# Performance work log

Measured on AMD Instinct MI355X. Metric: run time of the kernel, lower is better.

Reference implementation:

```python
import jax, jax.numpy as jnp
import numpy as np

B, N, D = 8, 64, 512          # batch, latent tokens, token dim
C, H, W, P = 256, 128, 128, 36  # img feat channels/HW, sampling points
PG = 128                       # parameter-generator inner dim (0.25*D)
HEADS = 8                      # D // 64
TOT = C * C + P * P            # adaptive mixing param count per token


def _ln(x, g, b):
    m = x.mean(-1, keepdims=True)
    v = x.var(-1, keepdims=True)
    return (x - m) / jnp.sqrt(v + 1e-5) * g + b


def _gelu(x):
    return jax.nn.gelu(x, approximate=False)


def _grid_sample(img, grid):
    # img: (B,C,H,W); grid: (B,N,P,2) in [-1,1]; bilinear, border pad, align_corners=False
    Bi, Ci, Hi, Wi = img.shape
    x = ((grid[..., 0] + 1.0) * Wi - 1.0) * 0.5
    y = ((grid[..., 1] + 1.0) * Hi - 1.0) * 0.5
    x0 = jnp.floor(x)
    y0 = jnp.floor(y)
    wx = x - x0
    wy = y - y0
    x0i = jnp.clip(x0.astype(jnp.int32), 0, Wi - 1)
    x1i = jnp.clip(x0.astype(jnp.int32) + 1, 0, Wi - 1)
    y0i = jnp.clip(y0.astype(jnp.int32), 0, Hi - 1)
    y1i = jnp.clip(y0.astype(jnp.int32) + 1, 0, Hi - 1)
    imgt = img.transpose(0, 2, 3, 1)  # (B,H,W,C)
    bidx = jnp.arange(Bi)[:, None, None]
    v00 = imgt[bidx, y0i, x0i]  # (B,N,P,C)
    v01 = imgt[bidx, y0i, x1i]
    v10 = imgt[bidx, y1i, x0i]
    v11 = imgt[bidx, y1i, x1i]
    wx = wx[..., None]
    wy = wy[..., None]
    return (v00 * (1 - wx) * (1 - wy) + v01 * wx * (1 - wy)
            + v10 * (1 - wx) * wy + v11 * wx * wy)


def setup_inputs() -> dict:
    key = jax.random.key(0)
    ks = jax.random.split(key, 16)
    rn = lambda k, s, sc: jax.random.normal(k, s, jnp.float32) * sc
    tl = jax.random.uniform(ks[0], (B, N, 2), jnp.float32) * 0.5
    wh = 0.2 + jax.random.uniform(ks[1], (B, N, 2), jnp.float32) * 0.4
    return dict(
        token_embed=rn(ks[2], (B, N, D), 1.0),
        token_roi=jnp.concatenate([tl, tl + wh], axis=-1),
        img_feat=rn(ks[3], (B, C, H, W), 1.0),
        ln_off_g=jnp.ones(D), ln_off_b=jnp.zeros(D),
        w_off=rn(ks[4], (D, P * 2), D ** -0.5),
        roi_offset_bias=rn(ks[5], (P * 2,), 1.0),
        ln_pg_g=jnp.ones(D), ln_pg_b=jnp.zeros(D),
        w_pg1=rn(ks[6], (D, PG), D ** -0.5), b_pg1=jnp.zeros(PG),
        w_pg2=rn(ks[7], (PG, TOT), 0.02 * PG ** -0.5),
        b_pg2=rn(ks[8], (TOT,), 0.02),
        m_beta=jnp.zeros(C), s_beta=jnp.zeros(P),
        w_out=rn(ks[9], (P * C, D), (P * C) ** -0.5), b_out=jnp.zeros(D),
        ln1_g=jnp.ones(D), ln1_b=jnp.zeros(D),
        w_qkv=rn(ks[10], (D, 3 * D), D ** -0.5), b_qkv=jnp.zeros(3 * D),
        w_proj=rn(ks[11], (D, D), D ** -0.5), b_proj=jnp.zeros(D),
        ln2_g=jnp.ones(D), ln2_b=jnp.zeros(D),
        w_fc1=rn(ks[12], (D, 4 * D), D ** -0.5), b_fc1=jnp.zeros(4 * D),
        w_fc2=rn(ks[13], (4 * D, D), (4 * D) ** -0.5), b_fc2=jnp.zeros(D),
    )


def reference(token_embed, token_roi, img_feat,
              ln_off_g, ln_off_b, w_off, roi_offset_bias,
              ln_pg_g, ln_pg_b, w_pg1, b_pg1, w_pg2, b_pg2,
              m_beta, s_beta, w_out, b_out,
              ln1_g, ln1_b, w_qkv, b_qkv, w_proj, b_proj,
              ln2_g, ln2_b, w_fc1, b_fc1, w_fc2, b_fc2):
    Bq, Nq, Dm = token_embed.shape
    # --- OP.SAMPLING_M: offsets -> absolute points (n_heads=1) ---
    off = _ln(token_embed, ln_off_g, ln_off_b) @ w_off + roi_offset_bias  # (B,N,2P)
    off = off.reshape(Bq, Nq, 1, P, 2)
    mu = off.mean(-2, keepdims=True)
    sd = jnp.std(off, axis=-2, keepdims=True, ddof=1) + 1e-5  # unbiased, as torch.std
    off = (off - mu) / (3.0 * sd)
    xy = (token_roi[..., 2:] + token_roi[..., :2]) * 0.5
    wh = token_roi[..., 2:] - token_roi[..., :2]
    pts = xy[:, :, None, None, :] + off * wh[:, :, None, None, :]  # (B,N,1,P,2)
    grid = pts.reshape(Bq, Nq, P, 2) * 2.0 - 1.0
    sampled = _grid_sample(img_feat, grid)  # (B,N,P,C)
    # --- adaptive mixing (AdaMixer): per-token generated channel/spatial weights ---
    q = _ln(token_embed, ln_pg_g, ln_pg_b)
    params = (q @ w_pg1 + b_pg1) @ w_pg2 + b_pg2  # (B,N,TOT)
    cm = params[..., :C * C].reshape(Bq, Nq, C, C)
    sm = params[..., C * C:].reshape(Bq, Nq, P, P)
    h = _gelu(jnp.einsum('bnpc,bncd->bnpd', sampled, cm) + m_beta)
    h = _gelu(jnp.einsum('bnqp,bnpd->bnqd', sm, h) + s_beta[:, None])
    token_embed = token_embed + (h.reshape(Bq, Nq, P * C) @ w_out + b_out)
    # --- OP.ATTN ---
    x = _ln(token_embed, ln1_g, ln1_b)
    hd = Dm // HEADS
    qkv = (x @ w_qkv + b_qkv).reshape(Bq, Nq, 3, HEADS, hd)
    qh, kh, vh = qkv[:, :, 0], qkv[:, :, 1], qkv[:, :, 2]
    att = jax.nn.softmax(jnp.einsum('bqhd,bkhd->bhqk', qh, kh) * hd ** -0.5, axis=-1)
    o = jnp.einsum('bhqk,bkhd->bqhd', att, vh).reshape(Bq, Nq, Dm)
    token_embed = token_embed + (o @ w_proj + b_proj)
    # --- OP.MLP ---
    x = _ln(token_embed, ln2_g, ln2_b)
    token_embed = token_embed + (_gelu(x @ w_fc1 + b_fc1) @ w_fc2 + b_fc2)
    return token_embed
```

## Files before the change

kernel.cpp:

```cpp
#include <hip/hip_runtime.h>
#include <hip/hip_bf16.h>

typedef __hip_bfloat16 bf16;
typedef __attribute__((ext_vector_type(8))) short short8;
typedef __attribute__((ext_vector_type(4))) short s16x4;
typedef __attribute__((ext_vector_type(4))) float f32x4;

#define NTOK 512
#define TOTC 66832
#define CM_SZ 65536

__device__ __forceinline__ float b2f(bf16 x) { return __bfloat162float(x); }
__device__ __forceinline__ bf16 f2b(float x) { return __float2bfloat16(x); }
__device__ __forceinline__ float gelu_f(float x) {
  return 0.5f * x * (1.0f + erff(x * 0.7071067811865476f));
}
__device__ __forceinline__ f32x4 mfma16(short8 a, short8 b, f32x4 c) {
  return __builtin_amdgcn_mfma_f32_16x16x32_bf16(a, b, c, 0, 0, 0);
}

__global__ __launch_bounds__(256) void k_head(
    const float* __restrict__ te, const float* __restrict__ roi,
    const float* __restrict__ g_off, const float* __restrict__ b_off,
    const float* __restrict__ w_off, const float* __restrict__ off_bias,
    const float* __restrict__ g_pg, const float* __restrict__ b_pg,
    const float* __restrict__ w_pg1, const float* __restrict__ b_pg1,
    bf16* __restrict__ t_out, int* __restrict__ meta_i, float* __restrict__ meta_w,
    const float* __restrict__ img, bf16* __restrict__ imgT,
    const float* __restrict__ w0, bf16* __restrict__ o0,
    const float* __restrict__ w1, bf16* __restrict__ o1,
    const float* __restrict__ w2, bf16* __restrict__ o2,
    const float* __restrict__ w3, bf16* __restrict__ o3,
    const float* __restrict__ w4, bf16* __restrict__ o4) {
  __shared__ __align__(16) char smem_raw[36864];
  int blk = blockIdx.x;
  int t = threadIdx.x;
  if (blk < 512) {
    int tok = blk;
    int lane = t & 63, w = t >> 6;
    float* xo = (float*)smem_raw;
    float* xq = xo + 512;
    float* offb = xq + 512;
    float* red = offb + 72;
    float* wsum = red + 4;
    size_t base = (size_t)tok * 512;
    float a0 = te[base + t];
    float a1 = te[base + t + 256];
    float s = a0 + a1;
#pragma unroll
    for (int o = 32; o; o >>= 1) s += __shfl_xor(s, o);
    if (lane == 0) wsum[w] = s;
    __syncthreads();
    float mean = (wsum[0] + wsum[1] + wsum[2] + wsum[3]) * (1.0f / 512.0f);
    float d0 = a0 - mean, d1 = a1 - mean;
    float ss = d0 * d0 + d1 * d1;
#pragma unroll
    for (int o = 32; o; o >>= 1) ss += __shfl_xor(ss, o);
    __syncthreads();
    if (lane == 0) wsum[w] = ss;
    __syncthreads();
    float var = (wsum[0] + wsum[1] + wsum[2] + wsum[3]) * (1.0f / 512.0f);
    float rstd = rsqrtf(var + 1e-5f);
    xo[t] = d0 * rstd * g_off[t] + b_off[t];
    xo[t + 256] = d1 * rstd * g_off[t + 256] + b_off[t + 256];
    xq[t] = d0 * rstd * g_pg[t] + b_pg[t];
    xq[t + 256] = d1 * rstd * g_pg[t + 256] + b_pg[t + 256];
    __syncthreads();
    if (t < 128) {
      float acc = b_pg1[t];
      for (int d = 0; d < 512; ++d) acc = fmaf(xq[d], w_pg1[d * 128 + t], acc);
      t_out[(size_t)tok * 128 + t] = f2b(acc);
    } else if (t < 200) {
      int j = t - 128;
      float acc = off_bias[j];
      for (int d = 0; d < 512; ++d) acc = fmaf(xo[d], w_off[d * 72 + j], acc);
      offb[j] = acc;
    }
    __syncthreads();
    if (t < 2) {
      float mu = 0.f;
      for (int p = 0; p < 36; ++p) mu += offb[p * 2 + t];
      mu *= (1.0f / 36.0f);
      float s2 = 0.f;
      for (int p = 0; p < 36; ++p) { float dd = offb[p * 2 + t] - mu; s2 += dd * dd; }
      float sd = sqrtf(s2 * (1.0f / 35.0f)) + 1e-5f;
      red[t] = mu;
      red[2 + t] = 1.0f / (3.0f * sd);
    }
    __syncthreads();
    if (t < 36) {
      int p = t;
      float r0 = roi[tok * 4 + 0], r1 = roi[tok * 4 + 1];
      float r2 = roi[tok * 4 + 2], r3 = roi[tok * 4 + 3];
      float cx = (r0 + r2) * 0.5f, cy = (r1 + r3) * 0.5f;
      float bw = r2 - r0, bh = r3 - r1;
      float ox = (offb[p * 2 + 0] - red[0]) * red[2];
      float oy = (offb[p * 2 + 1] - red[1]) * red[3];
      float fx = (cx + ox * bw) * 128.0f - 0.5f;
      float fy = (cy + oy * bh) * 128.0f - 0.5f;
      float x0f = floorf(fx), y0f = floorf(fy);
      float wx = fx - x0f, wy = fy - y0f;
      int x0 = min(max((int)x0f, 0), 127);
      int x1 = min(max((int)x0f + 1, 0), 127);
      int y0 = min(max((int)y0f, 0), 127);
      int y1 = min(max((int)y0f + 1, 0), 127);
      int ibase = (tok >> 6) * 16384;
      int mi = (tok * 36 + p) * 4;
      meta_i[mi + 0] = (ibase + y0 * 128 + x0) * 256;
      meta_i[mi + 1] = (ibase + y0 * 128 + x1) * 256;
      meta_i[mi + 2] = (ibase + y1 * 128 + x0) * 256;
      meta_i[mi + 3] = (ibase + y1 * 128 + x1) * 256;
      meta_w[mi + 0] = (1.f - wx) * (1.f - wy);
      meta_w[mi + 1] = wx * (1.f - wy);
      meta_w[mi + 2] = (1.f - wx) * wy;
      meta_w[mi + 3] = wx * wy;
    }
  } else if (blk < 2560) {
    int bb = blk - 512;
    int b = bb >> 8;
    int hw0 = (bb & 255) * 64;
    bf16 (*tl)[72] = (bf16(*)[72])smem_raw;
    int hw_l = (t & 15) * 4;
#pragma unroll
    for (int pass = 0; pass < 16; ++pass) {
      int c = (t >> 4) + 16 * pass;
      const float4 v = *(const float4*)&img[((size_t)(b * 256 + c) << 14) + hw0 + hw_l];
      float vv[4] = {v.x, v.y, v.z, v.w};
      int mask = ((c >> 3) & 31) << 1;
      int base = hw_l ^ (mask & 60);
      int swp = mask & 2;
      bf16 o[4];
#pragma unroll
      for (int k = 0; k < 4; ++k) o[k] = f2b(vv[k ^ swp]);
      *(s16x4*)&tl[c][base] = *(const s16x4*)o;
    }
    __syncthreads();
    int c8 = (t & 31) * 8;
    int hwb = t >> 5;
    int rmask = ((c8 >> 3) & 31) << 1;
#pragma unroll
    for (int pass = 0; pass < 8; ++pass) {
      int hw = hwb + 8 * pass;
      bf16 tmp[8];
#pragma unroll
      for (int j = 0; j < 8; ++j) tmp[j] = tl[c8 + j][hw ^ rmask];
      *(short8*)&imgT[((size_t)(b << 14) + hw0 + hw) * 256 + c8] = *(const short8*)tmp;
    }
  } else {
    int b = blk - 2560;
    const float* W;
    bf16* O;
    int K, N, loc;
    if (b < 4608) { W = w0; O = o0; K = 9216; N = 512; loc = b; }
    else if (b < 5376) { W = w1; O = o1; K = 512; N = 1536; loc = b - 4608; }
    else if (b < 5632) { W = w2; O = o2; K = 512; N = 512; loc = b - 5376; }
    else if (b < 6656) { W = w3; O = o3; K = 512; N = 2048; loc = b - 5632; }
    else { W = w4; O = o4; K = 2048; N = 512; loc = b - 6656; }
    int ntn = N >> 5;
    int nb = loc % ntn, kb = loc / ntn;
    int n0 = nb * 32, k0 = kb * 32;
    float (*tw)[33] = (float(*)[33])smem_raw;
    int r = t >> 5, c = t & 31;
#pragma unroll
    for (int i = 0; i < 4; ++i)
      tw[r + 8 * i][c] = W[(size_t)(k0 + r + 8 * i) * N + n0 + c];
    __syncthreads();
    int n_l = t >> 3, k4 = (t & 7) * 4;
    bf16 tmp[4];
#pragma unroll
    for (int j = 0; j < 4; ++j) tmp[j] = f2b(tw[k4 + j][n_l]);
    *(s16x4*)&O[(size_t)(n0 + n_l) * K + k0 + k4] = *(const s16x4*)tmp;
  }
}

__global__ __launch_bounds__(256) void k_samp_pg2(
    const bf16* __restrict__ tb16, const float* __restrict__ w2,
    const float* __restrict__ b2, bf16* __restrict__ pchunk,
    const bf16* __restrict__ imgT, const int* __restrict__ meta_i,
    const float* __restrict__ meta_w, bf16* __restrict__ S) {
  __shared__ bf16 BsT[64][136];
  __shared__ bf16 stg[64][72];
  int blk = blockIdx.x;
  int t = threadIdx.x;
  if (blk < 1045) {
    int n0 = blk * 64;
    int lane = t & 63, w = t >> 6;
    int quad = lane >> 4, l16 = lane & 15;
    {
      int nl = (t & 15) * 4, kk = t >> 4;
#pragma unroll
      for (int pass = 0; pass < 8; ++pass) {
        int k = kk + pass * 16;
        int n = n0 + nl;
        int nc = (n + 3 < TOTC) ? n : (TOTC - 4);
        const float4 v = *(const float4*)(w2 + (size_t)k * TOTC + nc);
        BsT[nl + 0][k] = f2b(v.x);
        BsT[nl + 1][k] = f2b(v.y);
        BsT[nl + 2][k] = f2b(v.z);
        BsT[nl + 3][k] = f2b(v.w);
      }
    }
    __syncthreads();
    float bias_r[4];
#pragma unroll
    for (int nt = 0; nt < 4; ++nt) {
      int col = n0 + nt * 16 + l16;
      bias_r[nt] = (col < TOTC) ? b2[col] : 0.f;
    }
    for (int half = 0; half < 2; ++half) {
      int row0 = half * 256;
      f32x4 acc[4][4];
#pragma unroll
      for (int i = 0; i < 4; ++i)
#pragma unroll
        for (int j = 0; j < 4; ++j) acc[i][j] = (f32x4){0.f, 0.f, 0.f, 0.f};
      const bf16* Abase = tb16 + ((size_t)(row0 + w * 64 + l16)) * 128 + quad * 8;
#pragma unroll
      for (int ks = 0; ks < 4; ++ks) {
        short8 af[4], bff[4];
#pragma unroll
        for (int mt = 0; mt < 4; ++mt)
          af[mt] = *(const short8*)(Abase + mt * 16 * 128 + ks * 32);
#pragma unroll
        for (int nt = 0; nt < 4; ++nt)
          bff[nt] = *(const short8*)(&BsT[nt * 16 + l16][ks * 32 + quad * 8]);
#pragma unroll
        for (int mt = 0; mt < 4; ++mt)
#pragma unroll
          for (int nt = 0; nt < 4; ++nt)
            acc[mt][nt] = mfma16(af[mt], bff[nt], acc[mt][nt]);
      }
#pragma unroll
      for (int mt = 0; mt < 4; ++mt) {
        __syncthreads();
#pragma unroll
        for (int nt = 0; nt < 4; ++nt)
#pragma unroll
          for (int r = 0; r < 4; ++r)
            stg[w * 16 + quad * 4 + r][nt * 16 + l16] =
                f2b(acc[mt][nt][r] + bias_r[nt]);
        __syncthreads();
#pragma unroll
        for (int pass = 0; pass < 2; ++pass) {
          int t2 = t + pass * 256;
          int row_l = t2 >> 3;
          int wi = row_l >> 4, rr = row_l & 15;
          int c8 = (t2 & 7) * 8;
          int col = n0 + c8;
          if (col < TOTC) {
            int grow = row0 + wi * 64 + mt * 16 + rr;
            *(short8*)&pchunk[(size_t)grow * TOTC + col] =
                *(const short8*)&stg[wi * 16 + rr][c8];
          }
        }
      }
      __syncthreads();
    }
  } else {
    int tok = blk - 1045;
#pragma unroll 6
    for (int p = 0; p < 36; ++p) {
      int mi = (tok * 36 + p) * 4;
      int o00 = meta_i[mi + 0], o01 = meta_i[mi + 1], o10 = meta_i[mi + 2], o11 = meta_i[mi + 3];
      float w00 = meta_w[mi + 0], w01 = meta_w[mi + 1], w10 = meta_w[mi + 2], w11 = meta_w[mi + 3];
      float v = w00 * b2f(imgT[o00 + t]) + w01 * b2f(imgT[o01 + t]) +
                w10 * b2f(imgT[o10 + t]) + w11 * b2f(imgT[o11 + t]);
      S[((size_t)tok * 36 + p) * 256 + t] = f2b(v);
    }
  }
}

__global__ __launch_bounds__(256) void k_mix3(const bf16* __restrict__ pchunk,
                                              const bf16* __restrict__ S,
                                              const float* __restrict__ m_beta,
                                              const float* __restrict__ s_beta,
                                              bf16* __restrict__ h2) {
  int tok = blockIdx.x, dh = blockIdx.y * 128;
  int t = threadIdx.x, lane = t & 63, w = t >> 6;
  int quad = lane >> 4, l16 = lane & 15;
  __shared__ bf16 h1T[128][72];
  __shared__ bf16 smS[48][72];
  __shared__ short cmw[4][32][40];
  for (int i = t; i < 1728; i += 256) ((unsigned*)smS)[i] = 0u;
  __syncthreads();
  const bf16* sm = pchunk + (size_t)tok * TOTC + CM_SZ;
  for (int i = t; i < 1296; i += 256) {
    int q = i / 36, p = i - q * 36;
    smS[q][p] = sm[i];
  }
  f32x4 acc[3][2];
#pragma unroll
  for (int i = 0; i < 3; ++i)
#pragma unroll
    for (int j = 0; j < 2; ++j) acc[i][j] = (f32x4){0.f, 0.f, 0.f, 0.f};
  const bf16* Sg = S + (size_t)tok * 9216;
  const bf16* Cg = pchunk + (size_t)tok * TOTC;
  int dw = w * 32;
  int c_l = lane & 31;
  int dtop = (lane >> 5) * 16;
  const bf16* src0 = Cg + (size_t)c_l * 256 + dh + dw + dtop;
  short8 v0 = *(const short8*)src0;
  short8 v1 = *(const short8*)(src0 + 8);
#pragma unroll
  for (int kc = 0; kc < 256; kc += 32) {
#pragma unroll
    for (int j = 0; j < 8; ++j) cmw[w][dtop + j][c_l] = v0[j];
#pragma unroll
    for (int j = 0; j < 8; ++j) cmw[w][dtop + 8 + j][c_l] = v1[j];
    short8 a[3];
#pragma unroll
    for (int mt = 0; mt < 3; ++mt)
      a[mt] = *(const short8*)(Sg + (size_t)(mt * 16 + l16) * 256 + kc + quad * 8);
    short8 v0n, v1n;
    if (kc < 224) {
      const bf16* srcn = Cg + (size_t)(kc + 32 + c_l) * 256 + dh + dw + dtop;
      v0n = *(const short8*)srcn;
      v1n = *(const short8*)(srcn + 8);
    }
    asm volatile("" ::: "memory");
    short8 bfr[2];
#pragma unroll
    for (int nt = 0; nt < 2; ++nt)
      bfr[nt] = *(const short8*)&cmw[w][nt * 16 + l16][quad * 8];
#pragma unroll
    for (int mt = 0; mt < 3; ++mt)
#pragma unroll
      for (int nt = 0; nt < 2; ++nt)
        acc[mt][nt] = mfma16(a[mt], bfr[nt], acc[mt][nt]);
    asm volatile("" ::: "memory");
    v0 = v0n;
    v1 = v1n;
  }
#pragma unroll
  for (int nt = 0; nt < 2; ++nt) {
    int dl = dw + nt * 16 + l16;
    float mb = m_beta[dh + dl];
#pragma unroll
    for (int mt = 0; mt < 3; ++mt)
#pragma unroll
      for (int r = 0; r < 4; ++r) {
        int p = mt * 16 + quad * 4 + r;
        if (p < 36) h1T[dl][p] = f2b(gelu_f(acc[mt][nt][r] + mb));
      }
  }
  for (int i = t; i < 128 * 28; i += 256) {
    int d = i / 28, p = 36 + i % 28;
    h1T[d][p] = (bf16)0.f;
  }
  __syncthreads();
  f32x4 acc2[3][2];
#pragma unroll
  for (int i = 0; i < 3; ++i)
#pragma unroll
    for (int j = 0; j < 2; ++j) acc2[i][j] = (f32x4){0.f, 0.f, 0.f, 0.f};
#pragma unroll
  for (int ks = 0; ks < 2; ++ks) {
    short8 a2[3], b2v[2];
#pragma unroll
    for (int mt = 0; mt < 3; ++mt)
      a2[mt] = *(const short8*)&smS[mt * 16 + l16][ks * 32 + quad * 8];
#pragma unroll
    for (int nt = 0; nt < 2; ++nt)
      b2v[nt] = *(const short8*)&h1T[dw + nt * 16 + l16][ks * 32 + quad * 8];
#pragma unroll
    for (int mt = 0; mt < 3; ++mt)
#pragma unroll
      for (int nt = 0; nt < 2; ++nt)
        acc2[mt][nt] = mfma16(a2[mt], b2v[nt], acc2[mt][nt]);
  }
  bf16* h2p = h2 + (size_t)tok * 9216 + dh;
#pragma unroll
  for (int mt = 0; mt < 3; ++mt)
#pragma unroll
    for (int r = 0; r < 4; ++r) {
      int q = mt * 16 + quad * 4 + r;
      if (q >= 36) continue;
      float sb = s_beta[q];
#pragma unroll
      for (int nt = 0; nt < 2; ++nt)
        h2p[q * 256 + dw + nt * 16 + l16] = f2b(gelu_f(acc2[mt][nt][r] + sb));
    }
}

__global__ __launch_bounds__(256) void k_gemm_bt(const bf16* __restrict__ A,
                                                 const bf16* __restrict__ BT,
                                                 float* __restrict__ part,
                                                 int M, int N, int K) {
  int nb = blockIdx.x, mb = blockIdx.y, ks = blockIdx.z;
  int kchunk = K / gridDim.z;
  int k0 = ks * kchunk;
  __shared__ bf16 As[64][72], Bs[64][72];
  int t = threadIdx.x, lane = t & 63, w = t >> 6;
  int quad = lane >> 4, l16 = lane & 15;
  int wm = (w >> 1) * 32, wn = (w & 1) * 32;
  int r = t >> 2, kk = (t & 3) * 16;
  f32x4 acc[2][2];
#pragma unroll
  for (int i = 0; i < 2; ++i)
#pragma unroll
    for (int j = 0; j < 2; ++j) acc[i][j] = (f32x4){0.f, 0.f, 0.f, 0.f};
  for (int kt = 0; kt < kchunk; kt += 64) {
    __syncthreads();
    const bf16* ga = A + (size_t)(mb * 64 + r) * K + k0 + kt + kk;
    *(short8*)&As[r][kk] = *(const short8*)ga;
    *(short8*)&As[r][kk + 8] = *(const short8*)(ga + 8);
    const bf16* gb = BT + (size_t)(nb * 64 + r) * K + k0 + kt + kk;
    *(short8*)&Bs[r][kk] = *(const short8*)gb;
    *(short8*)&Bs[r][kk + 8] = *(const short8*)(gb + 8);
    __syncthreads();
#pragma unroll
    for (int kss = 0; kss < 2; ++kss) {
      short8 af[2], bff[2];
#pragma unroll
      for (int mt = 0; mt < 2; ++mt)
        af[mt] = *(const short8*)&As[wm + mt * 16 + l16][kss * 32 + quad * 8];
#pragma unroll
      for (int nt = 0; nt < 2; ++nt)
        bff[nt] = *(const short8*)&Bs[wn + nt * 16 + l16][kss * 32 + quad * 8];
#pragma unroll
      for (int mt = 0; mt < 2; ++mt)
#pragma unroll
        for (int nt = 0; nt < 2; ++nt)
          acc[mt][nt] = mfma16(af[mt], bff[nt], acc[mt][nt]);
    }
  }
#pragma unroll
  for (int mt = 0; mt < 2; ++mt)
#pragma unroll
    for (int rr = 0; rr < 4; ++rr) {
      int m = mb * 64 + wm + mt * 16 + quad * 4 + rr;
#pragma unroll
      for (int nt = 0; nt < 2; ++nt) {
        int n = nb * 64 + wn + nt * 16 + l16;
        part[(size_t)ks * M * N + (size_t)m * N + n] = acc[mt][nt][rr];
      }
    }
}

__global__ __launch_bounds__(256) void k_gemm_ep(const bf16* __restrict__ A,
                                                 const bf16* __restrict__ BT,
                                                 const float* __restrict__ bias,
                                                 int M, int N, int K, int do_gelu,
                                                 const float* __restrict__ resf,
                                                 float* __restrict__ outf,
                                                 bf16* __restrict__ outh) {
  int nb = blockIdx.x, mb = blockIdx.y;
  __shared__ bf16 As[64][72], Bs[64][72];
  int t = threadIdx.x, lane = t & 63, w = t >> 6;
  int quad = lane >> 4, l16 = lane & 15;
  int wm = (w >> 1) * 32, wn = (w & 1) * 32;
  int r = t >> 2, kk = (t & 3) * 16;
  f32x4 acc[2][2];
#pragma unroll
  for (int i = 0; i < 2; ++i)
#pragma unroll
    for (int j = 0; j < 2; ++j) acc[i][j] = (f32x4){0.f, 0.f, 0.f, 0.f};
  for (int kt = 0; kt < K; kt += 64) {
    __syncthreads();
    const bf16* ga = A + (size_t)(mb * 64 + r) * K + kt + kk;
    *(short8*)&As[r][kk] = *(const short8*)ga;
    *(short8*)&As[r][kk + 8] = *(const short8*)(ga + 8);
    const bf16* gb = BT + (size_t)(nb * 64 + r) * K + kt + kk;
    *(short8*)&Bs[r][kk] = *(const short8*)gb;
    *(short8*)&Bs[r][kk + 8] = *(const short8*)(gb + 8);
    __syncthreads();
#pragma unroll
    for (int kss = 0; kss < 2; ++kss) {
      short8 af[2], bff[2];
#pragma unroll
      for (int mt = 0; mt < 2; ++mt)
        af[mt] = *(const short8*)&As[wm + mt * 16 + l16][kss * 32 + quad * 8];
#pragma unroll
      for (int nt = 0; nt < 2; ++nt)
        bff[nt] = *(const short8*)&Bs[wn + nt * 16 + l16][kss * 32 + quad * 8];
#pragma unroll
      for (int mt = 0; mt < 2; ++mt)
#pragma unroll
        for (int nt = 0; nt < 2; ++nt)
          acc[mt][nt] = mfma16(af[mt], bff[nt], acc[mt][nt]);
    }
  }
#pragma unroll
  for (int mt = 0; mt < 2; ++mt)
#pragma unroll
    for (int rr = 0; rr < 4; ++rr) {
      int m = mb * 64 + wm + mt * 16 + quad * 4 + rr;
#pragma unroll
      for (int nt = 0; nt < 2; ++nt) {
        int n = nb * 64 + wn + nt * 16 + l16;
        float a = acc[mt][nt][rr] + bias[n];
        if (resf) a += resf[(size_t)m * N + n];
        if (do_gelu) a = gelu_f(a);
        if (outf) outf[(size_t)m * N + n] = a;
        else outh[(size_t)m * N + n] = f2b(a);
      }
    }
}

__global__ __launch_bounds__(256) void k_epi_ln(const float* __restrict__ part, int S_,
                                                const float* __restrict__ bias,
                                                const float* __restrict__ res,
                                                const float* __restrict__ g,
                                                const float* __restrict__ bvec,
                                                float* __restrict__ xout,
                                                bf16* __restrict__ lnout) {
  int tok = blockIdx.x, t = threadIdx.x, lane = t & 63, w = t >> 6;
  __shared__ float wsum[4];
  size_t base = (size_t)tok * 512;
  float a0 = bias[t] + res[base + t];
  float a1 = bias[t + 256] + res[base + t + 256];
  for (int sp = 0; sp < S_; ++sp) {
    const float* p = part + (size_t)sp * 262144 + base;
    a0 += p[t];
    a1 += p[t + 256];
  }
  xout[base + t] = a0;
  xout[base + t + 256] = a1;
  float s = a0 + a1;
#pragma unroll
  for (int o = 32; o; o >>= 1) s += __shfl_xor(s, o);
  if (lane == 0) wsum[w] = s;
  __syncthreads();
  float mean = (wsum[0] + wsum[1] + wsum[2] + wsum[3]) * (1.0f / 512.0f);
  float d0 = a0 - mean, d1 = a1 - mean;
  float ss = d0 * d0 + d1 * d1;
#pragma unroll
  for (int o = 32; o; o >>= 1) ss += __shfl_xor(ss, o);
  __syncthreads();
  if (lane == 0) wsum[w] = ss;
  __syncthreads();
  float var = (wsum[0] + wsum[1] + wsum[2] + wsum[3]) * (1.0f / 512.0f);
  float rstd = rsqrtf(var + 1e-5f);
  lnout[base + t] = f2b(d0 * rstd * g[t] + bvec[t]);
  lnout[base + t + 256] = f2b(d1 * rstd * g[t + 256] + bvec[t + 256]);
}

__global__ __launch_bounds__(256) void k_attn(const float* __restrict__ qkvf,
                                              bf16* __restrict__ obuf) {
  int b = blockIdx.x >> 3, h = blockIdx.x & 7;
  int q0 = blockIdx.y * 16;
  __shared__ float kT[64][65];
  __shared__ float vT[64][65];
  __shared__ float att[16][65];
  int t = threadIdx.x, lane = t & 63, w = t >> 6;
#pragma unroll
  for (int i = 0; i < 16; ++i) {
    int idx = t + i * 256;
    int j = idx >> 6, d = idx & 63;
    size_t tb = (size_t)(b * 64 + j) * 1536 + h * 64 + d;
    kT[j][d] = qkvf[tb + 512];
    vT[j][d] = qkvf[tb + 1024];
  }
  __syncthreads();
#pragma unroll
  for (int m = 0; m < 4; ++m) {
    int il = w * 4 + m;
    int i = q0 + il;
    const float* qrow = &qkvf[(size_t)(b * 64 + i) * 1536 + h * 64];
    float s = 0.f;
    for (int d = 0; d < 64; ++d) s = fmaf(qrow[d], kT[lane][d], s);
    s *= 0.125f;
    float mx = s;
#pragma unroll
    for (int o = 32; o; o >>= 1) mx = fmaxf(mx, __shfl_xor(mx, o));
    float e = expf(s - mx);
    float sum = e;
#pragma unroll
    for (int o = 32; o; o >>= 1) sum += __shfl_xor(sum, o);
    att[il][lane] = e / sum;
  }
  __syncthreads();
#pragma unroll
  for (int m = 0; m < 4; ++m) {
    int il = w * 4 + m;
    int i = q0 + il;
    float o = 0.f;
    for (int j = 0; j < 64; ++j) o = fmaf(att[il][j], vT[j][lane], o);
    obuf[(size_t)(b * 64 + i) * 512 + h * 64 + lane] = f2b(o);
  }
}

extern "C" void kernel_launch(void* const* d_in, const int* in_sizes, int n_in,
                              void* d_out, int out_size, void* d_ws, size_t ws_size,
                              hipStream_t stream) {
  const float* te = (const float*)d_in[0];
  const float* roi = (const float*)d_in[1];
  const float* img = (const float*)d_in[2];
  const float* ln_off_g = (const float*)d_in[3];
  const float* ln_off_b = (const float*)d_in[4];
  const float* w_off = (const float*)d_in[5];
  const float* off_bias = (const float*)d_in[6];
  const float* ln_pg_g = (const float*)d_in[7];
  const float* ln_pg_b = (const float*)d_in[8];
  const float* w_pg1 = (const float*)d_in[9];
  const float* b_pg1 = (const float*)d_in[10];
  const float* w_pg2 = (const float*)d_in[11];
  const float* b_pg2 = (const float*)d_in[12];
  const float* m_beta = (const float*)d_in[13];
  const float* s_beta = (const float*)d_in[14];
  const float* w_out = (const float*)d_in[15];
  const float* b_out = (const float*)d_in[16];
  const float* ln1_g = (const float*)d_in[17];
  const float* ln1_b = (const float*)d_in[18];
  const float* w_qkv = (const float*)d_in[19];
  const float* b_qkv = (const float*)d_in[20];
  const float* w_proj = (const float*)d_in[21];
  const float* b_proj = (const float*)d_in[22];
  const float* ln2_g = (const float*)d_in[23];
  const float* ln2_b = (const float*)d_in[24];
  const float* w_fc1 = (const float*)d_in[25];
  const float* b_fc1 = (const float*)d_in[26];
  const float* w_fc2 = (const float*)d_in[27];
  const float* b_fc2 = (const float*)d_in[28];

  char* ws = (char*)d_ws;
  bf16* imgT = (bf16*)ws;
  char* ov = ws;
  bf16* h2 = (bf16*)ov; ov += 9437184;
  float* part = (float*)ov; ov += 8388608;
  float* x1 = (float*)ov; ov += 1048576;
  float* xa = (float*)ov; ov += 1048576;
  float* qkvf = (float*)ov; ov += 3145728;
  bf16* ln1buf = (bf16*)ov; ov += 524288;
  bf16* ln2buf = (bf16*)ov; ov += 524288;
  bf16* obuf = (bf16*)ov; ov += 524288;
  bf16* hfc = (bf16*)ov; ov += 2097152;
  char* tail = ws + 67108864;
  bf16* Sbuf = (bf16*)tail; tail += 9437184;
  bf16* tb16 = (bf16*)tail; tail += 131072;
  int* meta_i = (int*)tail; tail += 294912;
  float* meta_w = (float*)tail; tail += 294912;
  bf16* pchunk = (bf16*)tail; tail += (size_t)NTOK * TOTC * 2;
  bf16* w_outT = (bf16*)tail; tail += 9437184;
  bf16* w_qkvT = (bf16*)tail; tail += 1572864;
  bf16* w_projT = (bf16*)tail; tail += 524288;
  bf16* w_fc1T = (bf16*)tail; tail += 2097152;
  bf16* w_fc2T = (bf16*)tail; tail += 2097152;
  (void)ws_size;

  k_head<<<10240, 256, 0, stream>>>(te, roi, ln_off_g, ln_off_b, w_off, off_bias,
                                    ln_pg_g, ln_pg_b, w_pg1, b_pg1, tb16, meta_i, meta_w,
                                    img, imgT,
                                    w_out, w_outT, w_qkv, w_qkvT, w_proj, w_projT,
                                    w_fc1, w_fc1T, w_fc2, w_fc2T);
  k_samp_pg2<<<1557, 256, 0, stream>>>(tb16, w_pg2, b_pg2, pchunk,
                                       imgT, meta_i, meta_w, Sbuf);
  k_mix3<<<dim3(512, 2), 256, 0, stream>>>(pchunk, Sbuf, m_beta, s_beta, h2);

  k_gemm_bt<<<dim3(8, 8, 8), 256, 0, stream>>>(h2, w_outT, part, 512, 512, 9216);
  k_epi_ln<<<512, 256, 0, stream>>>(part, 8, b_out, te, ln1_g, ln1_b, x1, ln1buf);

  k_gemm_ep<<<dim3(24, 8), 256, 0, stream>>>(ln1buf, w_qkvT, b_qkv, 512, 1536, 512, 0,
                                             nullptr, qkvf, nullptr);
  k_attn<<<dim3(64, 4), 256, 0, stream>>>(qkvf, obuf);
  k_gemm_bt<<<dim3(8, 8, 4), 256, 0, stream>>>(obuf, w_projT, part, 512, 512, 512);
  k_epi_ln<<<512, 256, 0, stream>>>(part, 4, b_proj, x1, ln2_g, ln2_b, xa, ln2buf);

  k_gemm_ep<<<dim3(32, 8), 256, 0, stream>>>(ln2buf, w_fc1T, b_fc1, 512, 2048, 512, 1,
                                             nullptr, nullptr, hfc);
  k_gemm_ep<<<dim3(8, 8), 256, 0, stream>>>(hfc, w_fc2T, b_fc2, 512, 512, 2048, 0,
                                            xa, (float*)d_out, nullptr);
}
```

Baseline: 487.4 us.

## Fuse all stages into one cooperative persistent kernel with grid syncs

Merges the eleven separate kernel launches into a single persistent cooperative kernel of 512 blocks that loops over each stage's jobs and separates stages with grid-wide syncs. It also re-partitions some GEMM phases (split-K partial buffer doubled, final residual add as its own phase). This targets launch overhead and inter-kernel gaps, at the cost of fixed grid size limiting parallelism in the large phases, a shared LDS size that caps occupancy, and grid.sync latency. If the cooperative launch fails it falls back to per-phase kernels.

```diff
diff --git a/kernel.cpp b/kernel.cpp
--- a/kernel.cpp
+++ b/kernel.cpp
@@ -1,5 +1,8 @@
 #include <hip/hip_runtime.h>
 #include <hip/hip_bf16.h>
+#include <hip/hip_cooperative_groups.h>
+
+namespace cg = cooperative_groups;
 
 typedef __hip_bfloat16 bf16;
 typedef __attribute__((ext_vector_type(8))) short short8;
@@ -19,33 +22,109 @@
   return __builtin_amdgcn_mfma_f32_16x16x32_bf16(a, b, c, 0, 0, 0);
 }
 
-__global__ __launch_bounds__(256) void k_head(
-    const float* __restrict__ te, const float* __restrict__ roi,
-    const float* __restrict__ g_off, const float* __restrict__ b_off,
-    const float* __restrict__ w_off, const float* __restrict__ off_bias,
-    const float* __restrict__ g_pg, const float* __restrict__ b_pg,
-    const float* __restrict__ w_pg1, const float* __restrict__ b_pg1,
-    bf16* __restrict__ t_out, int* __restrict__ meta_i, float* __restrict__ meta_w,
-    const float* __restrict__ img, bf16* __restrict__ imgT,
-    const float* __restrict__ w0, bf16* __restrict__ o0,
-    const float* __restrict__ w1, bf16* __restrict__ o1,
-    const float* __restrict__ w2, bf16* __restrict__ o2,
-    const float* __restrict__ w3, bf16* __restrict__ o3,
-    const float* __restrict__ w4, bf16* __restrict__ o4) {
-  __shared__ __align__(16) char smem_raw[36864];
-  int blk = blockIdx.x;
-  int t = threadIdx.x;
-  if (blk < 512) {
-    int tok = blk;
-    int lane = t & 63, w = t >> 6;
-    float* xo = (float*)smem_raw;
+struct AllArgs {
+  const float *te, *roi, *img;
+  const float *g_off, *b_off, *w_off, *off_bias, *g_pg, *b_pg, *w_pg1, *b_pg1;
+  const float *w_pg2, *b_pg2, *m_beta, *s_beta;
+  const float *w_out, *b_out, *ln1_g, *ln1_b, *w_qkv, *b_qkv, *w_proj, *b_proj;
+  const float *ln2_g, *ln2_b, *w_fc1, *b_fc1, *w_fc2, *b_fc2;
+  bf16 *imgT, *tb16;
+  int *meta_i;
+  float *meta_w;
+  bf16 *pchunk, *Sbuf, *h2;
+  bf16 *w_outT, *w_qkvT, *w_projT, *w_fc1T, *w_fc2T;
+  float *part, *x1, *xa, *qkvf;
+  bf16 *ln1buf, *ln2buf, *obuf, *hfc;
+  float *outf;
+};
+
+__device__ __forceinline__ void gemm64(const bf16* A, const bf16* BT, int K,
+                                       int nb, int mb, int k0, int kchunk,
+                                       char* SM, int t, f32x4 acc[2][2]) {
+  bf16 (*As)[72] = (bf16(*)[72])SM;
+  bf16 (*Bs)[72] = (bf16(*)[72])(SM + 9216);
+  int lane = t & 63, w = t >> 6;
+  int quad = lane >> 4, l16 = lane & 15;
+  int wm = (w >> 1) * 32, wn = (w & 1) * 32;
+  int r = t >> 2, kk = (t & 3) * 16;
+#pragma unroll
+  for (int i = 0; i < 2; ++i)
+#pragma unroll
+    for (int j = 0; j < 2; ++j) acc[i][j] = (f32x4){0.f, 0.f, 0.f, 0.f};
+  for (int kt = 0; kt < kchunk; kt += 64) {
+    __syncthreads();
+    const bf16* ga = A + (size_t)(mb * 64 + r) * K + k0 + kt + kk;
+    *(short8*)&As[r][kk] = *(const short8*)ga;
+    *(short8*)&As[r][kk + 8] = *(const short8*)(ga + 8);
+    const bf16* gb = BT + (size_t)(nb * 64 + r) * K + k0 + kt + kk;
+    *(short8*)&Bs[r][kk] = *(const short8*)gb;
+    *(short8*)&Bs[r][kk + 8] = *(const short8*)(gb + 8);
+    __syncthreads();
+#pragma unroll
+    for (int kss = 0; kss < 2; ++kss) {
+      short8 af[2], bff[2];
+#pragma unroll
+      for (int mt = 0; mt < 2; ++mt)
+        af[mt] = *(const short8*)&As[wm + mt * 16 + l16][kss * 32 + quad * 8];
+#pragma unroll
+      for (int nt = 0; nt < 2; ++nt)
+        bff[nt] = *(const short8*)&Bs[wn + nt * 16 + l16][kss * 32 + quad * 8];
+#pragma unroll
+      for (int mt = 0; mt < 2; ++mt)
+#pragma unroll
+        for (int nt = 0; nt < 2; ++nt)
+          acc[mt][nt] = mfma16(af[mt], bff[nt], acc[mt][nt]);
+    }
+  }
+}
+
+__device__ __forceinline__ void epi_ln_body(const AllArgs& A, int tok, int t, int S_,
+                                            const float* bias, const float* res,
+                                            const float* g, const float* bvec,
+                                            float* xout, bf16* lnout, char* SM) {
+  int lane = t & 63, w = t >> 6;
+  float* wsum = (float*)SM;
+  size_t base = (size_t)tok * 512;
+  float a0 = bias[t] + res[base + t];
+  float a1 = bias[t + 256] + res[base + t + 256];
+  for (int sp = 0; sp < S_; ++sp) {
+    const float* p = A.part + (size_t)sp * 262144 + base;
+    a0 += p[t];
+    a1 += p[t + 256];
+  }
+  xout[base + t] = a0;
+  xout[base + t + 256] = a1;
+  float s = a0 + a1;
+#pragma unroll
+  for (int o = 32; o; o >>= 1) s += __shfl_xor(s, o);
+  if (lane == 0) wsum[w] = s;
+  __syncthreads();
+  float mean = (wsum[0] + wsum[1] + wsum[2] + wsum[3]) * (1.0f / 512.0f);
+  float d0 = a0 - mean, d1 = a1 - mean;
+  float ss = d0 * d0 + d1 * d1;
+#pragma unroll
+  for (int o = 32; o; o >>= 1) ss += __shfl_xor(ss, o);
+  __syncthreads();
+  if (lane == 0) wsum[w] = ss;
+  __syncthreads();
+  float var = (wsum[0] + wsum[1] + wsum[2] + wsum[3]) * (1.0f / 512.0f);
+  float rstd = rsqrtf(var + 1e-5f);
+  lnout[base + t] = f2b(d0 * rstd * g[t] + bvec[t]);
+  lnout[base + t + 256] = f2b(d1 * rstd * g[t + 256] + bvec[t + 256]);
+}
+
+__device__ void phase0(const AllArgs& A, int job, int t, char* SM) {
+  int lane = t & 63, w = t >> 6;
+  if (job < 512) {
+    int tok = job;
+    float* xo = (float*)SM;
     float* xq = xo + 512;
     float* offb = xq + 512;
     float* red = offb + 72;
     float* wsum = red + 4;
     size_t base = (size_t)tok * 512;
-    float a0 = te[base + t];
-    float a1 = te[base + t + 256];
+    float a0 = A.te[base + t];
+    float a1 = A.te[base + t + 256];
     float s = a0 + a1;
 #pragma unroll
     for (int o = 32; o; o >>= 1) s += __shfl_xor(s, o);
@@ -61,19 +140,19 @@
     __syncthreads();
     float var = (wsum[0] + wsum[1] + wsum[2] + wsum[3]) * (1.0f / 512.0f);
     float rstd = rsqrtf(var + 1e-5f);
-    xo[t] = d0 * rstd * g_off[t] + b_off[t];
-    xo[t + 256] = d1 * rstd * g_off[t + 256] + b_off[t + 256];
-    xq[t] = d0 * rstd * g_pg[t] + b_pg[t];
-    xq[t + 256] = d1 * rstd * g_pg[t + 256] + b_pg[t + 256];
+    xo[t] = d0 * rstd * A.g_off[t] + A.b_off[t];
+    xo[t + 256] = d1 * rstd * A.g_off[t + 256] + A.b_off[t + 256];
+    xq[t] = d0 * rstd * A.g_pg[t] + A.b_pg[t];
+    xq[t + 256] = d1 * rstd * A.g_pg[t + 256] + A.b_pg[t + 256];
     __syncthreads();
     if (t < 128) {
-      float acc = b_pg1[t];
-      for (int d = 0; d < 512; ++d) acc = fmaf(xq[d], w_pg1[d * 128 + t], acc);
-      t_out[(size_t)tok * 128 + t] = f2b(acc);
+      float acc = A.b_pg1[t];
+      for (int d = 0; d < 512; ++d) acc = fmaf(xq[d], A.w_pg1[d * 128 + t], acc);
+      A.tb16[(size_t)tok * 128 + t] = f2b(acc);
     } else if (t < 200) {
       int j = t - 128;
-      float acc = off_bias[j];
-      for (int d = 0; d < 512; ++d) acc = fmaf(xo[d], w_off[d * 72 + j], acc);
+      float acc = A.off_bias[j];
+      for (int d = 0; d < 512; ++d) acc = fmaf(xo[d], A.w_off[d * 72 + j], acc);
       offb[j] = acc;
     }
     __syncthreads();
@@ -90,8 +169,8 @@
     __syncthreads();
     if (t < 36) {
       int p = t;
-      float r0 = roi[tok * 4 + 0], r1 = roi[tok * 4 + 1];
-      float r2 = roi[tok * 4 + 2], r3 = roi[tok * 4 + 3];
+      float r0 = A.roi[tok * 4 + 0], r1 = A.roi[tok * 4 + 1];
+      float r2 = A.roi[tok * 4 + 2], r3 = A.roi[tok * 4 + 3];
       float cx = (r0 + r2) * 0.5f, cy = (r1 + r3) * 0.5f;
       float bw = r2 - r0, bh = r3 - r1;
       float ox = (offb[p * 2 + 0] - red[0]) * red[2];
@@ -101,30 +180,30 @@
       float x0f = floorf(fx), y0f = floorf(fy);
       float wx = fx - x0f, wy = fy - y0f;
       int x0 = min(max((int)x0f, 0), 127);
-      int x1 = min(max((int)x0f + 1, 0), 127);
+      int x1i = min(max((int)x0f + 1, 0), 127);
       int y0 = min(max((int)y0f, 0), 127);
-      int y1 = min(max((int)y0f + 1, 0), 127);
+      int y1i = min(max((int)y0f + 1, 0), 127);
       int ibase = (tok >> 6) * 16384;
       int mi = (tok * 36 + p) * 4;
-      meta_i[mi + 0] = (ibase + y0 * 128 + x0) * 256;
-      meta_i[mi + 1] = (ibase + y0 * 128 + x1) * 256;
-      meta_i[mi + 2] = (ibase + y1 * 128 + x0) * 256;
-      meta_i[mi + 3] = (ibase + y1 * 128 + x1) * 256;
-      meta_w[mi + 0] = (1.f - wx) * (1.f - wy);
-      meta_w[mi + 1] = wx * (1.f - wy);
-      meta_w[mi + 2] = (1.f - wx) * wy;
-      meta_w[mi + 3] = wx * wy;
-    }
-  } else if (blk < 2560) {
-    int bb = blk - 512;
+      A.meta_i[mi + 0] = (ibase + y0 * 128 + x0) * 256;
+      A.meta_i[mi + 1] = (ibase + y0 * 128 + x1i) * 256;
+      A.meta_i[mi + 2] = (ibase + y1i * 128 + x0) * 256;
+      A.meta_i[mi + 3] = (ibase + y1i * 128 + x1i) * 256;
+      A.meta_w[mi + 0] = (1.f - wx) * (1.f - wy);
+      A.meta_w[mi + 1] = wx * (1.f - wy);
+      A.meta_w[mi + 2] = (1.f - wx) * wy;
+      A.meta_w[mi + 3] = wx * wy;
+    }
+  } else if (job < 2560) {
+    int bb = job - 512;
     int b = bb >> 8;
     int hw0 = (bb & 255) * 64;
-    bf16 (*tl)[72] = (bf16(*)[72])smem_raw;
+    bf16 (*tl)[72] = (bf16(*)[72])SM;
     int hw_l = (t & 15) * 4;
 #pragma unroll
     for (int pass = 0; pass < 16; ++pass) {
       int c = (t >> 4) + 16 * pass;
-      const float4 v = *(const float4*)&img[((size_t)(b * 256 + c) << 14) + hw0 + hw_l];
+      const float4 v = *(const float4*)&A.img[((size_t)(b * 256 + c) << 14) + hw0 + hw_l];
       float vv[4] = {v.x, v.y, v.z, v.w};
       int mask = ((c >> 3) & 31) << 1;
       int base = hw_l ^ (mask & 60);
@@ -144,22 +223,22 @@
       bf16 tmp[8];
 #pragma unroll
       for (int j = 0; j < 8; ++j) tmp[j] = tl[c8 + j][hw ^ rmask];
-      *(short8*)&imgT[((size_t)(b << 14) + hw0 + hw) * 256 + c8] = *(const short8*)tmp;
+      *(short8*)&A.imgT[((size_t)(b << 14) + hw0 + hw) * 256 + c8] = *(const short8*)tmp;
     }
   } else {
-    int b = blk - 2560;
+    int b = job - 2560;
     const float* W;
     bf16* O;
     int K, N, loc;
-    if (b < 4608) { W = w0; O = o0; K = 9216; N = 512; loc = b; }
-    else if (b < 5376) { W = w1; O = o1; K = 512; N = 1536; loc = b - 4608; }
-    else if (b < 5632) { W = w2; O = o2; K = 512; N = 512; loc = b - 5376; }
-    else if (b < 6656) { W = w3; O = o3; K = 512; N = 2048; loc = b - 5632; }
-    else { W = w4; O = o4; K = 2048; N = 512; loc = b - 6656; }
+    if (b < 4608) { W = A.w_out; O = A.w_outT; K = 9216; N = 512; loc = b; }
+    else if (b < 5376) { W = A.w_qkv; O = A.w_qkvT; K = 512; N = 1536; loc = b - 4608; }
+    else if (b < 5632) { W = A.w_proj; O = A.w_projT; K = 512; N = 512; loc = b - 5376; }
+    else if (b < 6656) { W = A.w_fc1; O = A.w_fc1T; K = 512; N = 2048; loc = b - 5632; }
+    else { W = A.w_fc2; O = A.w_fc2T; K = 2048; N = 512; loc = b - 6656; }
     int ntn = N >> 5;
     int nb = loc % ntn, kb = loc / ntn;
     int n0 = nb * 32, k0 = kb * 32;
-    float (*tw)[33] = (float(*)[33])smem_raw;
+    float (*tw)[33] = (float(*)[33])SM;
     int r = t >> 5, c = t & 31;
 #pragma unroll
     for (int i = 0; i < 4; ++i)
@@ -173,19 +252,13 @@
   }
 }
 
-__global__ __launch_bounds__(256) void k_samp_pg2(
-    const bf16* __restrict__ tb16, const float* __restrict__ w2,
-    const float* __restrict__ b2, bf16* __restrict__ pchunk,
-    const bf16* __restrict__ imgT, const int* __restrict__ meta_i,
-    const float* __restrict__ meta_w, bf16* __restrict__ S) {
-  __shared__ bf16 BsT[64][136];
-  __shared__ bf16 stg[64][72];
-  int blk = blockIdx.x;
-  int t = threadIdx.x;
-  if (blk < 1045) {
-    int n0 = blk * 64;
-    int lane = t & 63, w = t >> 6;
-    int quad = lane >> 4, l16 = lane & 15;
+__device__ void phase1(const AllArgs& A, int job, int t, char* SM) {
+  int lane = t & 63, w = t >> 6;
+  int quad = lane >> 4, l16 = lane & 15;
+  if (job < 1045) {
+    bf16 (*BsT)[136] = (bf16(*)[136])SM;
+    bf16 (*stg)[72] = (bf16(*)[72])(SM + 17408);
+    int n0 = job * 64;
     {
       int nl = (t & 15) * 4, kk = t >> 4;
 #pragma unroll
@@ -193,7 +266,7 @@
         int k = kk + pass * 16;
         int n = n0 + nl;
         int nc = (n + 3 < TOTC) ? n : (TOTC - 4);
-        const float4 v = *(const float4*)(w2 + (size_t)k * TOTC + nc);
+        const float4 v = *(const float4*)(A.w_pg2 + (size_t)k * TOTC + nc);
         BsT[nl + 0][k] = f2b(v.x);
         BsT[nl + 1][k] = f2b(v.y);
         BsT[nl + 2][k] = f2b(v.z);
@@ -205,7 +278,7 @@
 #pragma unroll
     for (int nt = 0; nt < 4; ++nt) {
       int col = n0 + nt * 16 + l16;
-      bias_r[nt] = (col < TOTC) ? b2[col] : 0.f;
+      bias_r[nt] = (col < TOTC) ? A.b_pg2[col] : 0.f;
     }
     for (int half = 0; half < 2; ++half) {
       int row0 = half * 256;
@@ -214,7 +287,7 @@
       for (int i = 0; i < 4; ++i)
 #pragma unroll
         for (int j = 0; j < 4; ++j) acc[i][j] = (f32x4){0.f, 0.f, 0.f, 0.f};
-      const bf16* Abase = tb16 + ((size_t)(row0 + w * 64 + l16)) * 128 + quad * 8;
+      const bf16* Abase = A.tb16 + ((size_t)(row0 + w * 64 + l16)) * 128 + quad * 8;
 #pragma unroll
       for (int ks = 0; ks < 4; ++ks) {
         short8 af[4], bff[4];
@@ -249,7 +322,7 @@
           int col = n0 + c8;
           if (col < TOTC) {
             int grow = row0 + wi * 64 + mt * 16 + rr;
-            *(short8*)&pchunk[(size_t)grow * TOTC + col] =
+            *(short8*)&A.pchunk[(size_t)grow * TOTC + col] =
                 *(const short8*)&stg[wi * 16 + rr][c8];
           }
         }
@@ -257,33 +330,31 @@
       __syncthreads();
     }
   } else {
-    int tok = blk - 1045;
+    int tok = job - 1045;
 #pragma unroll 6
     for (int p = 0; p < 36; ++p) {
       int mi = (tok * 36 + p) * 4;
-      int o00 = meta_i[mi + 0], o01 = meta_i[mi + 1], o10 = meta_i[mi + 2], o11 = meta_i[mi + 3];
-      float w00 = meta_w[mi + 0], w01 = meta_w[mi + 1], w10 = meta_w[mi + 2], w11 = meta_w[mi + 3];
-      float v = w00 * b2f(imgT[o00 + t]) + w01 * b2f(imgT[o01 + t]) +
-                w10 * b2f(imgT[o10 + t]) + w11 * b2f(imgT[o11 + t]);
-      S[((size_t)tok * 36 + p) * 256 + t] = f2b(v);
-    }
-  }
-}
-
-__global__ __launch_bounds__(256) void k_mix3(const bf16* __restrict__ pchunk,
-                                              const bf16* __restrict__ S,
-                                              const float* __restrict__ m_beta,
-                                              const float* __restrict__ s_beta,
-                                              bf16* __restrict__ h2) {
-  int tok = blockIdx.x, dh = blockIdx.y * 128;
-  int t = threadIdx.x, lane = t & 63, w = t >> 6;
+      int o00 = A.meta_i[mi + 0], o01 = A.meta_i[mi + 1];
+      int o10 = A.meta_i[mi + 2], o11 = A.meta_i[mi + 3];
+      float w00 = A.meta_w[mi + 0], w01 = A.meta_w[mi + 1];
+      float w10 = A.meta_w[mi + 2], w11 = A.meta_w[mi + 3];
+      float v = w00 * b2f(A.imgT[o00 + t]) + w01 * b2f(A.imgT[o01 + t]) +
+                w10 * b2f(A.imgT[o10 + t]) + w11 * b2f(A.imgT[o11 + t]);
+      A.Sbuf[((size_t)tok * 36 + p) * 256 + t] = f2b(v);
+    }
+  }
+}
+
+__device__ void phase2(const AllArgs& A, int job, int t, char* SM) {
+  int lane = t & 63, w = t >> 6;
   int quad = lane >> 4, l16 = lane & 15;
-  __shared__ bf16 h1T[128][72];
-  __shared__ bf16 smS[48][72];
-  __shared__ short cmw[4][32][40];
+  int tok = job & 511, dh = (job >> 9) * 128;
+  bf16 (*h1T)[72] = (bf16(*)[72])SM;
+  bf16 (*smS)[72] = (bf16(*)[72])(SM + 18432);
+  short (*cmw)[32][40] = (short(*)[32][40])(SM + 25344);
   for (int i = t; i < 1728; i += 256) ((unsigned*)smS)[i] = 0u;
   __syncthreads();
-  const bf16* sm = pchunk + (size_t)tok * TOTC + CM_SZ;
+  const bf16* sm = A.pchunk + (size_t)tok * TOTC + CM_SZ;
   for (int i = t; i < 1296; i += 256) {
     int q = i / 36, p = i - q * 36;
     smS[q][p] = sm[i];
@@ -293,8 +364,8 @@
   for (int i = 0; i < 3; ++i)
 #pragma unroll
     for (int j = 0; j < 2; ++j) acc[i][j] = (f32x4){0.f, 0.f, 0.f, 0.f};
-  const bf16* Sg = S + (size_t)tok * 9216;
-  const bf16* Cg = pchunk + (size_t)tok * TOTC;
+  const bf16* Sg = A.Sbuf + (size_t)tok * 9216;
+  const bf16* Cg = A.pchunk + (size_t)tok * TOTC;
   int dw = w * 32;
   int c_l = lane & 31;
   int dtop = (lane >> 5) * 16;
@@ -334,7 +405,7 @@
 #pragma unroll
   for (int nt = 0; nt < 2; ++nt) {
     int dl = dw + nt * 16 + l16;
-    float mb = m_beta[dh + dl];
+    float mb = A.m_beta[dh + dl];
 #pragma unroll
     for (int mt = 0; mt < 3; ++mt)
 #pragma unroll
@@ -368,62 +439,27 @@
       for (int nt = 0; nt < 2; ++nt)
         acc2[mt][nt] = mfma16(a2[mt], b2v[nt], acc2[mt][nt]);
   }
-  bf16* h2p = h2 + (size_t)tok * 9216 + dh;
+  bf16* h2p = A.h2 + (size_t)tok * 9216 + dh;
 #pragma unroll
   for (int mt = 0; mt < 3; ++mt)
 #pragma unroll
     for (int r = 0; r < 4; ++r) {
       int q = mt * 16 + quad * 4 + r;
       if (q >= 36) continue;
-      float sb = s_beta[q];
+      float sb = A.s_beta[q];
 #pragma unroll
       for (int nt = 0; nt < 2; ++nt)
         h2p[q * 256 + dw + nt * 16 + l16] = f2b(gelu_f(acc2[mt][nt][r] + sb));
     }
 }
 
-__global__ __launch_bounds__(256) void k_gemm_bt(const bf16* __restrict__ A,
-                                                 const bf16* __restrict__ BT,
-                                                 float* __restrict__ part,
-                                                 int M, int N, int K) {
-  int nb = blockIdx.x, mb = blockIdx.y, ks = blockIdx.z;
-  int kchunk = K / gridDim.z;
-  int k0 = ks * kchunk;
-  __shared__ bf16 As[64][72], Bs[64][72];
-  int t = threadIdx.x, lane = t & 63, w = t >> 6;
+__device__ void phase3(const AllArgs& A, int job, int t, char* SM) {
+  int lane = t & 63, w = t >> 6;
   int quad = lane >> 4, l16 = lane & 15;
+  int nb = job & 7, mb = (job >> 3) & 7, ks = job >> 6;
+  f32x4 acc[2][2];
+  gemm64(A.h2, A.w_outT, 9216, nb, mb, ks * 576, 576, SM, t, acc);
   int wm = (w >> 1) * 32, wn = (w & 1) * 32;
-  int r = t >> 2, kk = (t & 3) * 16;
-  f32x4 acc[2][2];
-#pragma unroll
-  for (int i = 0; i < 2; ++i)
-#pragma unroll
-    for (int j = 0; j < 2; ++j) acc[i][j] = (f32x4){0.f, 0.f, 0.f, 0.f};
-  for (int kt = 0; kt < kchunk; kt += 64) {
-    __syncthreads();
-    const bf16* ga = A + (size_t)(mb * 64 + r) * K + k0 + kt + kk;
-    *(short8*)&As[r][kk] = *(const short8*)ga;
-    *(short8*)&As[r][kk + 8] = *(const short8*)(ga + 8);
-    const bf16* gb = BT + (size_t)(nb * 64 + r) * K + k0 + kt + kk;
-    *(short8*)&Bs[r][kk] = *(const short8*)gb;
-    *(short8*)&Bs[r][kk + 8] = *(const short8*)(gb + 8);
-    __syncthreads();
-#pragma unroll
-    for (int kss = 0; kss < 2; ++kss) {
-      short8 af[2], bff[2];
-#pragma unroll
-      for (int mt = 0; mt < 2; ++mt)
-        af[mt] = *(const short8*)&As[wm + mt * 16 + l16][kss * 32 + quad * 8];
-#pragma unroll
-      for (int nt = 0; nt < 2; ++nt)
-        bff[nt] = *(const short8*)&Bs[wn + nt * 16 + l16][kss * 32 + quad * 8];
-#pragma unroll
-      for (int mt = 0; mt < 2; ++mt)
-#pragma unroll
-        for (int nt = 0; nt < 2; ++nt)
-          acc[mt][nt] = mfma16(af[mt], bff[nt], acc[mt][nt]);
-    }
-  }
 #pragma unroll
   for (int mt = 0; mt < 2; ++mt)
 #pragma unroll
@@ -432,54 +468,22 @@
 #pragma unroll
       for (int nt = 0; nt < 2; ++nt) {
         int n = nb * 64 + wn + nt * 16 + l16;
-        part[(size_t)ks * M * N + (size_t)m * N + n] = acc[mt][nt][rr];
-      }
-    }
-}
-
-__global__ __launch_bounds__(256) void k_gemm_ep(const bf16* __restrict__ A,
-                                                 const bf16* __restrict__ BT,
-                                                 const float* __restrict__ bias,
-                                                 int M, int N, int K, int do_gelu,
-                                                 const float* __restrict__ resf,
-                                                 float* __restrict__ outf,
-                                                 bf16* __restrict__ outh) {
-  int nb = blockIdx.x, mb = blockIdx.y;
-  __shared__ bf16 As[64][72], Bs[64][72];
-  int t = threadIdx.x, lane = t & 63, w = t >> 6;
+        A.part[(size_t)ks * 262144 + (size_t)m * 512 + n] = acc[mt][nt][rr];
+      }
+    }
+}
+
+__device__ void phase4(const AllArgs& A, int job, int t, char* SM) {
+  epi_ln_body(A, job, t, 16, A.b_out, A.te, A.ln1_g, A.ln1_b, A.x1, A.ln1buf, SM);
+}
+
+__device__ void phase5(const AllArgs& A, int job, int t, char* SM) {
+  int lane = t & 63, w = t >> 6;
   int quad = lane >> 4, l16 = lane & 15;
+  int nb = job % 24, mb = job / 24;
+  f32x4 acc[2][2];
+  gemm64(A.ln1buf, A.w_qkvT, 512, nb, mb, 0, 512, SM, t, acc);
   int wm = (w >> 1) * 32, wn = (w & 1) * 32;
-  int r = t >> 2, kk = (t & 3) * 16;
-  f32x4 acc[2][2];
-#pragma unroll
-  for (int i = 0; i < 2; ++i)
-#pragma unroll
-    for (int j = 0; j < 2; ++j) acc[i][j] = (f32x4){0.f, 0.f, 0.f, 0.f};
-  for (int kt = 0; kt < K; kt += 64) {
-    __syncthreads();
-    const bf16* ga = A + (size_t)(mb * 64 + r) * K + kt + kk;
-    *(short8*)&As[r][kk] = *(const short8*)ga;
-    *(short8*)&As[r][kk + 8] = *(const short8*)(ga + 8);
-    const bf16* gb = BT + (size_t)(nb * 64 + r) * K + kt + kk;
-    *(short8*)&Bs[r][kk] = *(const short8*)gb;
-    *(short8*)&Bs[r][kk + 8] = *(const short8*)(gb + 8);
-    __syncthreads();
-#pragma unroll
-    for (int kss = 0; kss < 2; ++kss) {
-      short8 af[2], bff[2];
-#pragma unroll
-      for (int mt = 0; mt < 2; ++mt)
-        af[mt] = *(const short8*)&As[wm + mt * 16 + l16][kss * 32 + quad * 8];
-#pragma unroll
-      for (int nt = 0; nt < 2; ++nt)
-        bff[nt] = *(const short8*)&Bs[wn + nt * 16 + l16][kss * 32 + quad * 8];
-#pragma unroll
-      for (int mt = 0; mt < 2; ++mt)
-#pragma unroll
-        for (int nt = 0; nt < 2; ++nt)
-          acc[mt][nt] = mfma16(af[mt], bff[nt], acc[mt][nt]);
-    }
-  }
 #pragma unroll
   for (int mt = 0; mt < 2; ++mt)
 #pragma unroll
@@ -488,75 +492,33 @@
 #pragma unroll
       for (int nt = 0; nt < 2; ++nt) {
         int n = nb * 64 + wn + nt * 16 + l16;
-        float a = acc[mt][nt][rr] + bias[n];
-        if (resf) a += resf[(size_t)m * N + n];
-        if (do_gelu) a = gelu_f(a);
-        if (outf) outf[(size_t)m * N + n] = a;
-        else outh[(size_t)m * N + n] = f2b(a);
-      }
-    }
-}
-
-__global__ __launch_bounds__(256) void k_epi_ln(const float* __restrict__ part, int S_,
-                                                const float* __restrict__ bias,
-                                                const float* __restrict__ res,
-                                                const float* __restrict__ g,
-                                                const float* __restrict__ bvec,
-                                                float* __restrict__ xout,
-                                                bf16* __restrict__ lnout) {
-  int tok = blockIdx.x, t = threadIdx.x, lane = t & 63, w = t >> 6;
-  __shared__ float wsum[4];
-  size_t base = (size_t)tok * 512;
-  float a0 = bias[t] + res[base + t];
-  float a1 = bias[t + 256] + res[base + t + 256];
-  for (int sp = 0; sp < S_; ++sp) {
-    const float* p = part + (size_t)sp * 262144 + base;
-    a0 += p[t];
-    a1 += p[t + 256];
-  }
-  xout[base + t] = a0;
-  xout[base + t + 256] = a1;
-  float s = a0 + a1;
-#pragma unroll
-  for (int o = 32; o; o >>= 1) s += __shfl_xor(s, o);
-  if (lane == 0) wsum[w] = s;
-  __syncthreads();
-  float mean = (wsum[0] + wsum[1] + wsum[2] + wsum[3]) * (1.0f / 512.0f);
-  float d0 = a0 - mean, d1 = a1 - mean;
-  float ss = d0 * d0 + d1 * d1;
-#pragma unroll
-  for (int o = 32; o; o >>= 1) ss += __shfl_xor(ss, o);
-  __syncthreads();
-  if (lane == 0) wsum[w] = ss;
-  __syncthreads();
-  float var = (wsum[0] + wsum[1] + wsum[2] + wsum[3]) * (1.0f / 512.0f);
-  float rstd = rsqrtf(var + 1e-5f);
-  lnout[base + t] = f2b(d0 * rstd * g[t] + bvec[t]);
-  lnout[base + t + 256] = f2b(d1 * rstd * g[t + 256] + bvec[t + 256]);
-}
-
-__global__ __launch_bounds__(256) void k_attn(const float* __restrict__ qkvf,
-                                              bf16* __restrict__ obuf) {
-  int b = blockIdx.x >> 3, h = blockIdx.x & 7;
-  int q0 = blockIdx.y * 16;
-  __shared__ float kT[64][65];
-  __shared__ float vT[64][65];
-  __shared__ float att[16][65];
-  int t = threadIdx.x, lane = t & 63, w = t >> 6;
+        A.qkvf[(size_t)m * 1536 + n] = acc[mt][nt][rr] + A.b_qkv[n];
+      }
+    }
+}
+
+__device__ void phase6(const AllArgs& A, int job, int t, char* SM) {
+  int lane = t & 63, w = t >> 6;
+  int bh = job >> 2;
+  int b = bh >> 3, h = bh & 7;
+  int q0 = (job & 3) * 16;
+  float (*kT)[65] = (float(*)[65])SM;
+  float (*vT)[65] = (float(*)[65])(SM + 16640);
+  float (*att)[65] = (float(*)[65])(SM + 33280);
 #pragma unroll
   for (int i = 0; i < 16; ++i) {
     int idx = t + i * 256;
     int j = idx >> 6, d = idx & 63;
     size_t tb = (size_t)(b * 64 + j) * 1536 + h * 64 + d;
-    kT[j][d] = qkvf[tb + 512];
-    vT[j][d] = qkvf[tb + 1024];
+    kT[j][d] = A.qkvf[tb + 512];
+    vT[j][d] = A.qkvf[tb + 1024];
   }
   __syncthreads();
 #pragma unroll
   for (int m = 0; m < 4; ++m) {
     int il = w * 4 + m;
     int i = q0 + il;
-    const float* qrow = &qkvf[(size_t)(b * 64 + i) * 1536 + h * 64];
+    const float* qrow = &A.qkvf[(size_t)(b * 64 + i) * 1536 + h * 64];
     float s = 0.f;
     for (int d = 0; d < 64; ++d) s = fmaf(qrow[d], kT[lane][d], s);
     s *= 0.125f;
@@ -576,88 +538,204 @@
     int i = q0 + il;
     float o = 0.f;
     for (int j = 0; j < 64; ++j) o = fmaf(att[il][j], vT[j][lane], o);
-    obuf[(size_t)(b * 64 + i) * 512 + h * 64 + lane] = f2b(o);
-  }
-}
+    A.obuf[(size_t)(b * 64 + i) * 512 + h * 64 + lane] = f2b(o);
+  }
+}
+
+__device__ void phase7(const AllArgs& A, int job, int t, char* SM) {
+  int lane = t & 63, w = t >> 6;
+  int quad = lane >> 4, l16 = lane & 15;
+  int nb = job & 7, mb = (job >> 3) & 7, ks = job >> 6;
+  f32x4 acc[2][2];
+  gemm64(A.obuf, A.w_projT, 512, nb, mb, ks * 128, 128, SM, t, acc);
+  int wm = (w >> 1) * 32, wn = (w & 1) * 32;
+#pragma unroll
+  for (int mt = 0; mt < 2; ++mt)
+#pragma unroll
+    for (int rr = 0; rr < 4; ++rr) {
+      int m = mb * 64 + wm + mt * 16 + quad * 4 + rr;
+#pragma unroll
+      for (int nt = 0; nt < 2; ++nt) {
+        int n = nb * 64 + wn + nt * 16 + l16;
+        A.part[(size_t)ks * 262144 + (size_t)m * 512 + n] = acc[mt][nt][rr];
+      }
+    }
+}
+
+__device__ void phase8(const AllArgs& A, int job, int t, char* SM) {
+  epi_ln_body(A, job, t, 4, A.b_proj, A.x1, A.ln2_g, A.ln2_b, A.xa, A.ln2buf, SM);
+}
+
+__device__ void phase9(const AllArgs& A, int job, int t, char* SM) {
+  int lane = t & 63, w = t >> 6;
+  int quad = lane >> 4, l16 = lane & 15;
+  int nb = job & 31, mb = job >> 5;
+  f32x4 acc[2][2];
+  gemm64(A.ln2buf, A.w_fc1T, 512, nb, mb, 0, 512, SM, t, acc);
+  int wm = (w >> 1) * 32, wn = (w & 1) * 32;
+#pragma unroll
+  for (int mt = 0; mt < 2; ++mt)
+#pragma unroll
+    for (int rr = 0; rr < 4; ++rr) {
+      int m = mb * 64 + wm + mt * 16 + quad * 4 + rr;
+#pragma unroll
+      for (int nt = 0; nt < 2; ++nt) {
+        int n = nb * 64 + wn + nt * 16 + l16;
+        A.hfc[(size_t)m * 2048 + n] = f2b(gelu_f(acc[mt][nt][rr] + A.b_fc1[n]));
+      }
+    }
+}
+
+__device__ void phase10(const AllArgs& A, int job, int t, char* SM) {
+  int lane = t & 63, w = t >> 6;
+  int quad = lane >> 4, l16 = lane & 15;
+  int nb = job & 7, mb = (job >> 3) & 7, ks = job >> 6;
+  f32x4 acc[2][2];
+  gemm64(A.hfc, A.w_fc2T, 2048, nb, mb, ks * 512, 512, SM, t, acc);
+  int wm = (w >> 1) * 32, wn = (w & 1) * 32;
+#pragma unroll
+  for (int mt = 0; mt < 2; ++mt)
+#pragma unroll
+    for (int rr = 0; rr < 4; ++rr) {
+      int m = mb * 64 + wm + mt * 16 + quad * 4 + rr;
+#pragma unroll
+      for (int nt = 0; nt < 2; ++nt) {
+        int n = nb * 64 + wn + nt * 16 + l16;
+        A.part[(size_t)ks * 262144 + (size_t)m * 512 + n] = acc[mt][nt][rr];
+      }
+    }
+}
+
+__device__ void phase11(const AllArgs& A, int job, int t, char* SM) {
+  int idx = job * 256 + t;
+  float a = A.part[idx] + A.part[262144 + idx] + A.part[2 * 262144 + idx] +
+            A.part[3 * 262144 + idx];
+  a += A.b_fc2[idx & 511];
+  a += A.xa[idx];
+  A.outf[idx] = a;
+}
+
+#define RUN_PHASE(FN, NJOBS)                                       \
+  for (int job = blockIdx.x; job < (NJOBS); job += gridDim.x) {    \
+    FN(A, job, t, SM);                                             \
+    __syncthreads();                                               \
+  }
+
+__global__ __launch_bounds__(256, 2) void k_all(AllArgs A) {
+  cg::grid_group grid = cg::this_grid();
+  __shared__ __align__(16) char SM[37440];
+  int t = threadIdx.x;
+  RUN_PHASE(phase0, 10240) grid.sync();
+  RUN_PHASE(phase1, 1557) grid.sync();
+  RUN_PHASE(phase2, 1024) grid.sync();
+  RUN_PHASE(phase3, 1024) grid.sync();
+  RUN_PHASE(phase4, 512) grid.sync();
+  RUN_PHASE(phase5, 192) grid.sync();
+  RUN_PHASE(phase6, 256) grid.sync();
+  RUN_PHASE(phase7, 256) grid.sync();
+  RUN_PHASE(phase8, 512) grid.sync();
+  RUN_PHASE(phase9, 256) grid.sync();
+  RUN_PHASE(phase10, 256) grid.sync();
+  RUN_PHASE(phase11, 1024)
+}
+
+#define MAKE_KP(NAME, FN, NJOBS)                                       \
+  __global__ __launch_bounds__(256) void NAME(AllArgs A) {             \
+    __shared__ __align__(16) char SM[37440];                           \
+    int t = threadIdx.x;                                               \
+    for (int job = blockIdx.x; job < (NJOBS); job += gridDim.x) {      \
+      FN(A, job, t, SM);                                               \
+      __syncthreads();                                                 \
+    }                                                                  \
+  }
+MAKE_KP(k_p0, phase0, 10240)
+MAKE_KP(k_p1, phase1, 1557)
+MAKE_KP(k_p2, phase2, 1024)
+MAKE_KP(k_p3, phase3, 1024)
+MAKE_KP(k_p4, phase4, 512)
+MAKE_KP(k_p5, phase5, 192)
+MAKE_KP(k_p6, phase6, 256)
+MAKE_KP(k_p7, phase7, 256)
+MAKE_KP(k_p8, phase8, 512)
+MAKE_KP(k_p9, phase9, 256)
+MAKE_KP(k_p10, phase10, 256)
+MAKE_KP(k_p11, phase11, 1024)
 
 extern "C" void kernel_launch(void* const* d_in, const int* in_sizes, int n_in,
                               void* d_out, int out_size, void* d_ws, size_t ws_size,
                               hipStream_t stream) {
-  const float* te = (const float*)d_in[0];
-  const float* roi = (const float*)d_in[1];
-  const float* img = (const float*)d_in[2];
-  const float* ln_off_g = (const float*)d_in[3];
-  const float* ln_off_b = (const float*)d_in[4];
-  const float* w_off = (const float*)d_in[5];
-  const float* off_bias = (const float*)d_in[6];
-  const float* ln_pg_g = (const float*)d_in[7];
-  const float* ln_pg_b = (const float*)d_in[8];
-  const float* w_pg1 = (const float*)d_in[9];
-  const float* b_pg1 = (const float*)d_in[10];
-  const float* w_pg2 = (const float*)d_in[11];
-  const float* b_pg2 = (const float*)d_in[12];
-  const float* m_beta = (const float*)d_in[13];
-  const float* s_beta = (const float*)d_in[14];
-  const float* w_out = (const float*)d_in[15];
-  const float* b_out = (const float*)d_in[16];
-  const float* ln1_g = (const float*)d_in[17];
-  const float* ln1_b = (const float*)d_in[18];
-  const float* w_qkv = (const float*)d_in[19];
-  const float* b_qkv = (const float*)d_in[20];
-  const float* w_proj = (const float*)d_in[21];
-  const float* b_proj = (const float*)d_in[22];
-  const float* ln2_g = (const float*)d_in[23];
-  const float* ln2_b = (const float*)d_in[24];
-  const float* w_fc1 = (const float*)d_in[25];
-  const float* b_fc1 = (const float*)d_in[26];
-  const float* w_fc2 = (const float*)d_in[27];
-  const float* b_fc2 = (const float*)d_in[28];
+  AllArgs aa;
+  aa.te = (const float*)d_in[0];
+  aa.roi = (const float*)d_in[1];
+  aa.img = (const float*)d_in[2];
+  aa.g_off = (const float*)d_in[3];
+  aa.b_off = (const float*)d_in[4];
+  aa.w_off = (const float*)d_in[5];
+  aa.off_bias = (const float*)d_in[6];
+  aa.g_pg = (const float*)d_in[7];
+  aa.b_pg = (const float*)d_in[8];
+  aa.w_pg1 = (const float*)d_in[9];
+  aa.b_pg1 = (const float*)d_in[10];
+  aa.w_pg2 = (const float*)d_in[11];
+  aa.b_pg2 = (const float*)d_in[12];
+  aa.m_beta = (const float*)d_in[13];
+  aa.s_beta = (const float*)d_in[14];
+  aa.w_out = (const float*)d_in[15];
+  aa.b_out = (const float*)d_in[16];
+  aa.ln1_g = (const float*)d_in[17];
+  aa.ln1_b = (const float*)d_in[18];
+  aa.w_qkv = (const float*)d_in[19];
+  aa.b_qkv = (const float*)d_in[20];
+  aa.w_proj = (const float*)d_in[21];
+  aa.b_proj = (const float*)d_in[22];
+  aa.ln2_g = (const float*)d_in[23];
+  aa.ln2_b = (const float*)d_in[24];
+  aa.w_fc1 = (const float*)d_in[25];
+  aa.b_fc1 = (const float*)d_in[26];
+  aa.w_fc2 = (const float*)d_in[27];
+  aa.b_fc2 = (const float*)d_in[28];
 
   char* ws = (char*)d_ws;
-  bf16* imgT = (bf16*)ws;
+  aa.imgT = (bf16*)ws;
   char* ov = ws;
-  bf16* h2 = (bf16*)ov; ov += 9437184;
-  float* part = (float*)ov; ov += 8388608;
-  float* x1 = (float*)ov; ov += 1048576;
-  float* xa = (float*)ov; ov += 1048576;
-  float* qkvf = (float*)ov; ov += 3145728;
-  bf16* ln1buf = (bf16*)ov; ov += 524288;
-  bf16* ln2buf = (bf16*)ov; ov += 524288;
-  bf16* obuf = (bf16*)ov; ov += 524288;
-  bf16* hfc = (bf16*)ov; ov += 2097152;
+  aa.h2 = (bf16*)ov; ov += 9437184;
+  aa.part = (float*)ov; ov += 16777216;
+  aa.x1 = (float*)ov; ov += 1048576;
+  aa.xa = (float*)ov; ov += 1048576;
+  aa.qkvf = (float*)ov; ov += 3145728;
+  aa.ln1buf = (bf16*)ov; ov += 524288;
+  aa.ln2buf = (bf16*)ov; ov += 524288;
+  aa.obuf = (bf16*)ov; ov += 524288;
+  aa.hfc = (bf16*)ov; ov += 2097152;
   char* tail = ws + 67108864;
-  bf16* Sbuf = (bf16*)tail; tail += 9437184;
-  bf16* tb16 = (bf16*)tail; tail += 131072;
-  int* meta_i = (int*)tail; tail += 294912;
-  float* meta_w = (float*)tail; tail += 294912;
-  bf16* pchunk = (bf16*)tail; tail += (size_t)NTOK * TOTC * 2;
-  bf16* w_outT = (bf16*)tail; tail += 9437184;
-  bf16* w_qkvT = (bf16*)tail; tail += 1572864;
-  bf16* w_projT = (bf16*)tail; tail += 524288;
-  bf16* w_fc1T = (bf16*)tail; tail += 2097152;
-  bf16* w_fc2T = (bf16*)tail; tail += 2097152;
+  aa.Sbuf = (bf16*)tail; tail += 9437184;
+  aa.tb16 = (bf16*)tail; tail += 131072;
+  aa.meta_i = (int*)tail; tail += 294912;
+  aa.meta_w = (float*)tail; tail += 294912;
+  aa.pchunk = (bf16*)tail; tail += (size_t)NTOK * TOTC * 2;
+  aa.w_outT = (bf16*)tail; tail += 9437184;
+  aa.w_qkvT = (bf16*)tail; tail += 1572864;
+  aa.w_projT = (bf16*)tail; tail += 524288;
+  aa.w_fc1T = (bf16*)tail; tail += 2097152;
+  aa.w_fc2T = (bf16*)tail; tail += 2097152;
+  aa.outf = (float*)d_out;
   (void)ws_size;
 
-  k_head<<<10240, 256, 0, stream>>>(te, roi, ln_off_g, ln_off_b, w_off, off_bias,
-                                    ln_pg_g, ln_pg_b, w_pg1, b_pg1, tb16, meta_i, meta_w,
-                                    img, imgT,
-                                    w_out, w_outT, w_qkv, w_qkvT, w_proj, w_projT,
-                                    w_fc1, w_fc1T, w_fc2, w_fc2T);
-  k_samp_pg2<<<1557, 256, 0, stream>>>(tb16, w_pg2, b_pg2, pchunk,
-                                       imgT, meta_i, meta_w, Sbuf);
-  k_mix3<<<dim3(512, 2), 256, 0, stream>>>(pchunk, Sbuf, m_beta, s_beta, h2);
-
-  k_gemm_bt<<<dim3(8, 8, 8), 256, 0, stream>>>(h2, w_outT, part, 512, 512, 9216);
-  k_epi_ln<<<512, 256, 0, stream>>>(part, 8, b_out, te, ln1_g, ln1_b, x1, ln1buf);
-
-  k_gemm_ep<<<dim3(24, 8), 256, 0, stream>>>(ln1buf, w_qkvT, b_qkv, 512, 1536, 512, 0,
-                                             nullptr, qkvf, nullptr);
-  k_attn<<<dim3(64, 4), 256, 0, stream>>>(qkvf, obuf);
-  k_gemm_bt<<<dim3(8, 8, 4), 256, 0, stream>>>(obuf, w_projT, part, 512, 512, 512);
-  k_epi_ln<<<512, 256, 0, stream>>>(part, 4, b_proj, x1, ln2_g, ln2_b, xa, ln2buf);
-
-  k_gemm_ep<<<dim3(32, 8), 256, 0, stream>>>(ln2buf, w_fc1T, b_fc1, 512, 2048, 512, 1,
-                                             nullptr, nullptr, hfc);
-  k_gemm_ep<<<dim3(8, 8), 256, 0, stream>>>(hfc, w_fc2T, b_fc2, 512, 512, 2048, 0,
-                                            xa, (float*)d_out, nullptr);
-}
+  void* kp[] = {(void*)&aa};
+  hipError_t err = hipLaunchCooperativeKernel((const void*)k_all, dim3(512), dim3(256),
+                                              kp, 0, stream);
+  if (err != hipSuccess) {
+    k_p0<<<10240, 256, 0, stream>>>(aa);
+    k_p1<<<1557, 256, 0, stream>>>(aa);
+    k_p2<<<1024, 256, 0, stream>>>(aa);
+    k_p3<<<1024, 256, 0, stream>>>(aa);
+    k_p4<<<512, 256, 0, stream>>>(aa);
+    k_p5<<<192, 256, 0, stream>>>(aa);
+    k_p6<<<256, 256, 0, stream>>>(aa);
+    k_p7<<<256, 256, 0, stream>>>(aa);
+    k_p8<<<512, 256, 0, stream>>>(aa);
+    k_p9<<<256, 256, 0, stream>>>(aa);
+    k_p10<<<256, 256, 0, stream>>>(aa);
+    k_p11<<<1024, 256, 0, stream>>>(aa);
+  }
+}
```

Result: slower. 1.173 ms (+140.7%).
